# Optimization experiments

Hardware: AMD Instinct MI355X
Metric: run time of the kernel (lower is better)

Reference implementation:

```python
import jax, jax.numpy as jnp
import numpy as np
from jax import lax

T, B, D = 1024, 32, 1024


def setup_inputs() -> dict:
    key = jax.random.key(0)
    k1, k2, k3, k4 = jax.random.split(key, 4)
    xav = (6.0 / (D + D)) ** 0.5  # xavier_uniform bound
    return {
        "x": jax.random.normal(k1, (T, B, D), dtype=jnp.float32),
        "h0": jnp.zeros((B, D), dtype=jnp.float32),
        "W_alpha": jax.random.uniform(k2, (D, D), minval=-xav, maxval=xav, dtype=jnp.float32),
        "d_alpha": jnp.full((D,), 0.1, dtype=jnp.float32),
        "b_alpha": jnp.full((D,), 2.0, dtype=jnp.float32),
        "W_x": jax.random.uniform(k3, (D, D), minval=-xav, maxval=xav, dtype=jnp.float32),
        "b_v": jnp.zeros((D,), dtype=jnp.float32),
    }


def reference(x, h0, W_alpha, d_alpha, b_alpha, W_x, b_v):
    # Precompute batched GEMMs once (x_t @ W.T), as in the original.
    alpha_x = jnp.einsum("tbd,ed->tbe", x, W_alpha)          # [T,B,D]
    v = jnp.tanh(jnp.einsum("tbd,ed->tbe", x, W_x) + b_v)    # [T,B,D]

    def step(h_prev, inp):
        ax_t, v_t = inp
        alpha = jax.nn.sigmoid(ax_t + d_alpha * h_prev + b_alpha)
        h_new = alpha * h_prev + (1.0 - alpha) * v_t
        out = h_new * h_new * jax.nn.sigmoid(h_new)  # h * silu(h)
        return h_new, (h_new, out)

    _, (hs, outs) = lax.scan(step, h0, (alpha_x, v))
    h = jnp.concatenate([h0[None], hs], axis=0)  # [T+1,B,D]
    return outs, h
```

## Files before the change

kernel.cpp:

```cpp
#include <hip/hip_runtime.h>
#include <hip/hip_bf16.h>
#include <stdint.h>

#define TT 1024
#define BB 32
#define DD 1024
#define MROWS (TT*BB)
#define NCOLS (2*DD)
#define KDIM  (DD)
#define BK 64
#define SS (BB*DD)

typedef __attribute__((ext_vector_type(8))) short short8;
typedef __attribute__((ext_vector_type(4))) float f32x4;

__device__ __forceinline__ float bf2f(uint16_t u){
  union { uint32_t u; float f; } c; c.u = ((uint32_t)u) << 16; return c.f;
}
__device__ __forceinline__ uint16_t f2bf(float f){
  union { float f; uint32_t u; } c; c.f = f;
  uint32_t u = c.u;
  u += 0x7FFFu + ((u >> 16) & 1u);
  return (uint16_t)(u >> 16);
}
__device__ __forceinline__ float tanh_fast(float x){
  return 1.f - 2.f/(1.f + __expf(2.f*x));
}
__device__ __forceinline__ float sigmoid_fast(float x){
  return __builtin_amdgcn_rcpf(1.f + __expf(-x));
}

__global__ __launch_bounds__(256) void cvt_x_kernel(const float* __restrict__ x,
                                                    uint16_t* __restrict__ xb, int n4){
  int i = blockIdx.x * 256 + threadIdx.x;
  int stride = gridDim.x * 256;
  for (; i < n4; i += stride){
    float4 f = ((const float4*)x)[i];
    ushort4 o;
    o.x = f2bf(f.x); o.y = f2bf(f.y); o.z = f2bf(f.z); o.w = f2bf(f.w);
    ((ushort4*)xb)[i] = o;
  }
}

__global__ __launch_bounds__(256) void cvt_w_kernel(const float* __restrict__ Wa,
                                                    const float* __restrict__ Wx,
                                                    uint16_t* __restrict__ wc){
  int i = blockIdx.x * 256 + threadIdx.x;
  const int c    = i >> 8;
  const int col4 = i & 255;
  const int e = ((c >> 5) << 4) | (c & 15);
  const int s = (c >> 4) & 1;
  const float* src = (s ? Wx : Wa) + (size_t)e*DD + col4*4;
  float4 f = *(const float4*)src;
  ushort4 o;
  o.x = f2bf(f.x); o.y = f2bf(f.y); o.z = f2bf(f.z); o.w = f2bf(f.w);
  ((ushort4*)wc)[i] = o;
}

__global__ __launch_bounds__(256) void gemm_dual(const uint16_t* __restrict__ xb,
                                                 const uint16_t* __restrict__ wc,
                                                 const float* __restrict__ bv,
                                                 uint32_t* __restrict__ av){
  __shared__ __align__(16) uint16_t As[128*BK];
  __shared__ __align__(16) uint16_t Bs[128*BK];
  const int tid  = threadIdx.x;
  const int lane = tid & 63;
  const int w    = tid >> 6;
  const int wm   = w >> 1, wn = w & 1;

  const int bid  = blockIdx.x;
  const int bsw  = (bid & 7) * 512 + (bid >> 3);
  const int bn   = (bsw & 15) << 7;
  const int bm   = (bsw >> 4) << 7;

  f32x4 acc[4][4] = {};

  const int sr = lane >> 3;
  const int srcoff = ((lane & 7) ^ sr) * 8;

  const int fr = lane & 15;
  const int fq = lane >> 4;
  int aaddr[2][4], baddr[2][4];
  #pragma unroll
  for (int kh = 0; kh < 2; ++kh){
    #pragma unroll
    for (int m = 0; m < 4; ++m){
      int ra = wm*64 + m*16 + fr;
      int pa = ((kh << 2) | fq) ^ (ra & 7);
      aaddr[kh][m] = ra*(BK*2) + pa*16;
      int rb = wn*64 + m*16 + fr;
      int pb = ((kh << 2) | fq) ^ (rb & 7);
      baddr[kh][m] = rb*(BK*2) + pb*16;
    }
  }

  for (int k0 = 0; k0 < KDIM; k0 += BK){
    #pragma unroll
    for (int c = 0; c < 4; ++c){
      const int rbase = w*32 + c*8;
      const uint16_t* gA = xb + (size_t)(bm + rbase + sr)*KDIM + k0 + srcoff;
      __builtin_amdgcn_global_load_lds((const __attribute__((address_space(1))) void*)gA,
                                       (__attribute__((address_space(3))) void*)(&As[rbase*BK]),
                                       16, 0, 0);
      const uint16_t* gB = wc + (size_t)(bn + rbase + sr)*KDIM + k0 + srcoff;
      __builtin_amdgcn_global_load_lds((const __attribute__((address_space(1))) void*)gB,
                                       (__attribute__((address_space(3))) void*)(&Bs[rbase*BK]),
                                       16, 0, 0);
    }
    __syncthreads();

    short8 aF[2][4], bF[2][4];
    #pragma unroll
    for (int kh = 0; kh < 2; ++kh){
      #pragma unroll
      for (int m = 0; m < 4; ++m){
        aF[kh][m] = *(const short8*)((const char*)As + aaddr[kh][m]);
        bF[kh][m] = *(const short8*)((const char*)Bs + baddr[kh][m]);
      }
    }
    #pragma unroll
    for (int kh = 0; kh < 2; ++kh)
      #pragma unroll
      for (int m = 0; m < 4; ++m)
        #pragma unroll
        for (int n = 0; n < 4; ++n)
          acc[m][n] = __builtin_amdgcn_mfma_f32_16x16x32_bf16(aF[kh][m], bF[kh][n], acc[m][n], 0, 0, 0);

    __syncthreads();
  }

  const int ebase = (bn + wn*64) >> 1;
  #pragma unroll
  for (int p = 0; p < 2; ++p){
    const int e = ebase + p*16 + fr;
    const float bvn = bv[e];
    #pragma unroll
    for (int m = 0; m < 4; ++m){
      #pragma unroll
      for (int j = 0; j < 4; ++j){
        const int row = bm + wm*64 + m*16 + fq*4 + j;
        const float a  = acc[m][2*p][j];
        const float vt = tanh_fast(acc[m][2*p+1][j] + bvn);
        const int t = row >> 5, b = row & 31;
        av[(size_t)t*SS + (size_t)b*DD + e] = (uint32_t)f2bf(a) | ((uint32_t)f2bf(vt) << 16);
      }
    }
  }
}

#define SCAN_STEP(u, tcur)                                        \
  {                                                               \
    const float a_ = bf2f((uint16_t)(u));                         \
    const float v_ = bf2f((uint16_t)((u) >> 16));                 \
    const float al_ = sigmoid_fast(a_ + da*h + ba);               \
    h = al_*(h - v_) + v_;                                        \
    const float sg_ = sigmoid_fast(h);                            \
    __builtin_nontemporal_store(h*h*sg_, &outs[(size_t)(tcur)*SS + idx]); \
    __builtin_nontemporal_store(h, &houts[(size_t)((tcur)+1)*SS + idx]);  \
  }

__global__ __launch_bounds__(64) void scan_kernel(const uint32_t* __restrict__ av,
                                                  const float* __restrict__ h0,
                                                  const float* __restrict__ d_alpha,
                                                  const float* __restrict__ b_alpha,
                                                  float* __restrict__ outs,
                                                  float* __restrict__ houts){
  const int idx = blockIdx.x * 64 + threadIdx.x;
  const int e = idx & (DD-1);
  const float da = d_alpha[e];
  const float ba = b_alpha[e];
  float h = h0[idx];
  __builtin_nontemporal_store(h, &houts[idx]);

  uint32_t bufA[32], bufB[32];
  #pragma unroll
  for (int j = 0; j < 32; ++j) bufA[j] = av[(size_t)j*SS + idx];

  for (int t0 = 0; t0 < TT; t0 += 64){
    #pragma unroll
    for (int j = 0; j < 32; ++j) bufB[j] = av[(size_t)(t0+32+j)*SS + idx];
    #pragma unroll
    for (int j = 0; j < 32; ++j) SCAN_STEP(bufA[j], t0 + j);
    if (t0 + 64 < TT){
      #pragma unroll
      for (int j = 0; j < 32; ++j) bufA[j] = av[(size_t)(t0+64+j)*SS + idx];
    }
    #pragma unroll
    for (int j = 0; j < 32; ++j) SCAN_STEP(bufB[j], t0 + 32 + j);
  }
}

extern "C" void kernel_launch(void* const* d_in, const int* in_sizes, int n_in,
                              void* d_out, int out_size, void* d_ws, size_t ws_size,
                              hipStream_t stream){
  const float* x  = (const float*)d_in[0];
  const float* h0 = (const float*)d_in[1];
  const float* Wa = (const float*)d_in[2];
  const float* da = (const float*)d_in[3];
  const float* ba = (const float*)d_in[4];
  const float* Wx = (const float*)d_in[5];
  const float* bv = (const float*)d_in[6];

  float* outs  = (float*)d_out;
  float* houts = outs + (size_t)TT*BB*DD;

  uint8_t* ws = (uint8_t*)d_ws;
  uint16_t* wcb = (uint16_t*)ws;
  uint16_t* xb  = (uint16_t*)(ws + (size_t)NCOLS*KDIM*2);
  uint32_t* av  = (uint32_t*)(ws + (size_t)NCOLS*KDIM*2 + (size_t)MROWS*KDIM*2);

  hipLaunchKernelGGL(cvt_w_kernel, dim3(2048), dim3(256), 0, stream, Wa, Wx, wcb);
  hipLaunchKernelGGL(cvt_x_kernel, dim3(2048), dim3(256), 0, stream, x, xb, MROWS*KDIM/4);
  hipLaunchKernelGGL(gemm_dual, dim3((NCOLS/128)*(MROWS/128)), dim3(256), 0, stream,
                     xb, wcb, bv, av);
  hipLaunchKernelGGL(scan_kernel, dim3(SS/64), dim3(64), 0, stream,
                     av, h0, da, ba, outs, houts);
}
```

Baseline: 294.7 us.

## Restructure dual GEMM into 256x256 tiles with double-buffered LDS pipeline

The GEMM block tile grows from 128x128 to 256x256 with 512 threads (8 waves, 2x4 layout). Operand tiles are double-buffered in 128KB of LDS, and the next k-tile's async global->LDS loads are issued in four phases interleaved with the MFMA work, using explicit barriers, waitcnts and setprio. The goal is to hide global load latency and raise arithmetic intensity per byte loaded. In exchange, LDS use and register pressure go up a lot, and the manual synchronisation is fragile.

```diff
diff --git a/kernel.cpp b/kernel.cpp
--- a/kernel.cpp
+++ b/kernel.cpp
@@ -8,7 +8,6 @@
 #define MROWS (TT*BB)
 #define NCOLS (2*DD)
 #define KDIM  (DD)
-#define BK 64
 #define SS (BB*DD)
 
 typedef __attribute__((ext_vector_type(8))) short short8;
@@ -57,77 +56,97 @@
   ((ushort4*)wc)[i] = o;
 }
 
-__global__ __launch_bounds__(256) void gemm_dual(const uint16_t* __restrict__ xb,
-                                                 const uint16_t* __restrict__ wc,
-                                                 const float* __restrict__ bv,
-                                                 uint32_t* __restrict__ av){
-  __shared__ __align__(16) uint16_t As[128*BK];
-  __shared__ __align__(16) uint16_t Bs[128*BK];
+__global__ __launch_bounds__(512, 2) void gemm_dual(const uint16_t* __restrict__ xb,
+                                                    const uint16_t* __restrict__ wc,
+                                                    const float* __restrict__ bv,
+                                                    uint32_t* __restrict__ av){
+  __shared__ __align__(16) uint16_t lds[65536];
+  char* ldsc = (char*)lds;
+
   const int tid  = threadIdx.x;
   const int lane = tid & 63;
   const int w    = tid >> 6;
-  const int wm   = w >> 1, wn = w & 1;
-
-  const int bid  = blockIdx.x;
-  const int bsw  = (bid & 7) * 512 + (bid >> 3);
-  const int bn   = (bsw & 15) << 7;
-  const int bm   = (bsw >> 4) << 7;
-
-  f32x4 acc[4][4] = {};
-
-  const int sr = lane >> 3;
-  const int srcoff = ((lane & 7) ^ sr) * 8;
-
-  const int fr = lane & 15;
-  const int fq = lane >> 4;
-  int aaddr[2][4], baddr[2][4];
-  #pragma unroll
-  for (int kh = 0; kh < 2; ++kh){
-    #pragma unroll
-    for (int m = 0; m < 4; ++m){
-      int ra = wm*64 + m*16 + fr;
-      int pa = ((kh << 2) | fq) ^ (ra & 7);
-      aaddr[kh][m] = ra*(BK*2) + pa*16;
-      int rb = wn*64 + m*16 + fr;
-      int pb = ((kh << 2) | fq) ^ (rb & 7);
-      baddr[kh][m] = rb*(BK*2) + pb*16;
-    }
-  }
-
-  for (int k0 = 0; k0 < KDIM; k0 += BK){
-    #pragma unroll
-    for (int c = 0; c < 4; ++c){
-      const int rbase = w*32 + c*8;
-      const uint16_t* gA = xb + (size_t)(bm + rbase + sr)*KDIM + k0 + srcoff;
-      __builtin_amdgcn_global_load_lds((const __attribute__((address_space(1))) void*)gA,
-                                       (__attribute__((address_space(3))) void*)(&As[rbase*BK]),
-                                       16, 0, 0);
-      const uint16_t* gB = wc + (size_t)(bn + rbase + sr)*KDIM + k0 + srcoff;
-      __builtin_amdgcn_global_load_lds((const __attribute__((address_space(1))) void*)gB,
-                                       (__attribute__((address_space(3))) void*)(&Bs[rbase*BK]),
-                                       16, 0, 0);
-    }
-    __syncthreads();
-
-    short8 aF[2][4], bF[2][4];
+  const int wm   = w >> 2;
+  const int wn   = w & 3;
+  const int fr   = lane & 15;
+  const int fq   = lane >> 4;
+
+  const int bid = blockIdx.x;
+  const int bsw = (bid & 7) * 128 + (bid >> 3);
+  const int bm  = (bsw >> 3) << 8;
+  const int bn  = (bsw & 7) << 8;
+
+  f32x4 acc[8][4] = {};
+
+  const int srow = tid >> 3;
+  const int soff = ((tid & 7) ^ (srow & 7)) * 8;
+
+  #define STAGE(kt, q) { \
+    const uint16_t* src_ = ((q) < 2) ? xb : wc; \
+    const int gbase_ = ((q) < 2) ? bm : bn; \
+    const int region_ = ((q) < 2) ? 0 : 65536; \
+    const int rb0_ = ((q) & 1) * 128; \
+    const int k0_ = (kt) * 64; \
+    _Pragma("unroll") \
+    for (int c_ = 0; c_ < 2; ++c_){ \
+      const uint16_t* g_ = src_ + (size_t)(gbase_ + rb0_ + c_*64 + srow)*KDIM + k0_ + soff; \
+      char* d_ = ldsc + region_ + ((kt) & 1)*32768 + (rb0_ + c_*64 + w*8)*128; \
+      __builtin_amdgcn_global_load_lds((const __attribute__((address_space(1))) void*)g_, \
+                                       (__attribute__((address_space(3))) void*)d_, 16, 0, 0); \
+    } \
+  }
+
+  STAGE(0,0) STAGE(0,1) STAGE(0,2) STAGE(0,3)
+  asm volatile("s_waitcnt vmcnt(0)" ::: "memory");
+  __builtin_amdgcn_s_barrier();
+
+  for (int t = 0; t < 16; ++t){
+    const int nbuf = (t & 1) * 32768;
+    const int aB0 = nbuf + (wm*128 + fr)*128;
+    const int bB0 = 65536 + nbuf + (wn*64 + fr)*128;
+    int aK[2], bK[2];
     #pragma unroll
     for (int kh = 0; kh < 2; ++kh){
-      #pragma unroll
-      for (int m = 0; m < 4; ++m){
-        aF[kh][m] = *(const short8*)((const char*)As + aaddr[kh][m]);
-        bF[kh][m] = *(const short8*)((const char*)Bs + baddr[kh][m]);
-      }
-    }
-    #pragma unroll
-    for (int kh = 0; kh < 2; ++kh)
-      #pragma unroll
-      for (int m = 0; m < 4; ++m)
-        #pragma unroll
-        for (int n = 0; n < 4; ++n)
-          acc[m][n] = __builtin_amdgcn_mfma_f32_16x16x32_bf16(aF[kh][m], bF[kh][n], acc[m][n], 0, 0, 0);
-
-    __syncthreads();
-  }
+      const int ps = ((kh*4 + fq) ^ (fr & 7)) * 16;
+      aK[kh] = aB0 + ps;
+      bK[kh] = bB0 + ps;
+    }
+
+    #define PHASE(q) { \
+      short8 aF[4][2], bF[2][2]; \
+      _Pragma("unroll") \
+      for (int m = 0; m < 4; ++m) \
+        _Pragma("unroll") \
+        for (int kh = 0; kh < 2; ++kh) \
+          aF[m][kh] = *(const short8*)(ldsc + aK[kh] + (((q)&1)*8192 + m*2048)); \
+      _Pragma("unroll") \
+      for (int n = 0; n < 2; ++n) \
+        _Pragma("unroll") \
+        for (int kh = 0; kh < 2; ++kh) \
+          bF[n][kh] = *(const short8*)(ldsc + bK[kh] + (((q)>>1)*4096 + n*2048)); \
+      if (t < 15) STAGE(t+1, q) \
+      __builtin_amdgcn_s_barrier(); \
+      asm volatile("s_waitcnt lgkmcnt(0)" ::: "memory"); \
+      __builtin_amdgcn_sched_barrier(0); \
+      __builtin_amdgcn_s_setprio(1); \
+      _Pragma("unroll") \
+      for (int m = 0; m < 4; ++m) \
+        _Pragma("unroll") \
+        for (int n = 0; n < 2; ++n) \
+          _Pragma("unroll") \
+          for (int kh = 0; kh < 2; ++kh) \
+            acc[((q)&1)*4+m][((q)>>1)*2+n] = \
+              __builtin_amdgcn_mfma_f32_16x16x32_bf16(aF[m][kh], bF[n][kh], \
+                                                      acc[((q)&1)*4+m][((q)>>1)*2+n], 0, 0, 0); \
+      __builtin_amdgcn_s_setprio(0); \
+      if ((q) == 3) asm volatile("s_waitcnt vmcnt(0)" ::: "memory"); \
+      __builtin_amdgcn_s_barrier(); \
+    }
+
+    PHASE(0) PHASE(1) PHASE(2) PHASE(3)
+    #undef PHASE
+  }
+  #undef STAGE
 
   const int ebase = (bn + wn*64) >> 1;
   #pragma unroll
@@ -135,14 +154,14 @@
     const int e = ebase + p*16 + fr;
     const float bvn = bv[e];
     #pragma unroll
-    for (int m = 0; m < 4; ++m){
+    for (int m = 0; m < 8; ++m){
       #pragma unroll
       for (int j = 0; j < 4; ++j){
-        const int row = bm + wm*64 + m*16 + fq*4 + j;
+        const int row = bm + wm*128 + m*16 + fq*4 + j;
         const float a  = acc[m][2*p][j];
         const float vt = tanh_fast(acc[m][2*p+1][j] + bvn);
-        const int t = row >> 5, b = row & 31;
-        av[(size_t)t*SS + (size_t)b*DD + e] = (uint32_t)f2bf(a) | ((uint32_t)f2bf(vt) << 16);
+        const int tt = row >> 5, b = row & 31;
+        av[(size_t)tt*SS + (size_t)b*DD + e] = (uint32_t)f2bf(a) | ((uint32_t)f2bf(vt) << 16);
       }
     }
   }
@@ -211,7 +230,7 @@
 
   hipLaunchKernelGGL(cvt_w_kernel, dim3(2048), dim3(256), 0, stream, Wa, Wx, wcb);
   hipLaunchKernelGGL(cvt_x_kernel, dim3(2048), dim3(256), 0, stream, x, xb, MROWS*KDIM/4);
-  hipLaunchKernelGGL(gemm_dual, dim3((NCOLS/128)*(MROWS/128)), dim3(256), 0, stream,
+  hipLaunchKernelGGL(gemm_dual, dim3((NCOLS/256)*(MROWS/256)), dim3(512), 0, stream,
                      xb, wcb, bv, av);
   hipLaunchKernelGGL(scan_kernel, dim3(SS/64), dim3(64), 0, stream,
                      av, h0, da, ba, outs, houts);
```

Result: faster. 273.2 us (-7.3%).
